# Performance work log

Hardware: AMD Instinct MI355X
Metric: run time of the kernel (lower is better)

Reference implementation:

```python
import jax, jax.numpy as jnp
import numpy as np

A_CONST = 0.1
B_CONST = 0.2
C_CONST = 0.8

INPUT_SIZE = 1024
HIDDEN_SIZE = 2048
BATCH = 32768
SIGMA = 0.02


def acti_func(x, a, b, c):
    # piecewise: a*(1 - x/b) for x<=b ; 0 for b<x<c ; a*(x-c)/(1-c) for x>=c
    low = -a * x / b + a
    high = a * x / (1.0 - c) + a * c / (c - 1.0)
    return jnp.where(x <= b, low, jnp.where(x >= c, high, jnp.zeros_like(x)))


def setup_inputs() -> dict:
    key = jax.random.key(0)
    ks = jax.random.split(key, 4)
    x = jax.random.normal(ks[0], (BATCH, INPUT_SIZE), dtype=jnp.float32)
    W0 = jax.random.normal(ks[1], (INPUT_SIZE, HIDDEN_SIZE), dtype=jnp.float32) * SIGMA
    b0 = jnp.zeros((HIDDEN_SIZE,), dtype=jnp.float32)
    W1 = jax.random.normal(ks[2], (HIDDEN_SIZE, HIDDEN_SIZE), dtype=jnp.float32) * SIGMA
    b1 = jnp.zeros((HIDDEN_SIZE,), dtype=jnp.float32)
    W2 = jax.random.normal(ks[3], (HIDDEN_SIZE, 1), dtype=jnp.float32) * SIGMA
    b2 = jnp.zeros((1,), dtype=jnp.float32)
    return {"x": x, "W0": W0, "b0": b0, "W1": W1, "b1": b1, "W2": W2, "b2": b2}


def reference(x, W0, b0, W1, b1, W2, b2):
    h = jax.nn.elu(x @ W0 + b0)
    h = jax.nn.elu(h @ W1 + b1)
    out = jax.nn.sigmoid(h @ W2 + b2)  # [B, 1]
    alpha = acti_func(out, A_CONST, B_CONST, C_CONST)
    return out, alpha
```

## Files before the change

### kernel.cpp

```cpp
#include <hip/hip_runtime.h>
#include <hip/hip_bf16.h>
#include <stdint.h>

typedef unsigned short u16;
typedef __bf16 bf16x8 __attribute__((ext_vector_type(8)));
typedef float floatx4 __attribute__((ext_vector_type(4)));

__device__ __forceinline__ u16 f2bf(float f) {
  union { float f; unsigned u; } c; c.f = f;
  unsigned r = c.u + 0x7fffu + ((c.u >> 16) & 1u);
  return (u16)(r >> 16);
}

__device__ __forceinline__ void load_lds16(const void* g, void* l) {
  __builtin_amdgcn_global_load_lds(
      (const __attribute__((address_space(1))) void*)g,
      (__attribute__((address_space(3))) void*)l,
      16, 0, 0);
}

__global__ void cast_f32_bf16(const float4* __restrict__ src, ushort4* __restrict__ dst, int n4) {
  int i = blockIdx.x * blockDim.x + threadIdx.x;
  if (i >= n4) return;
  float4 f = src[i];
  ushort4 u;
  u.x = f2bf(f.x); u.y = f2bf(f.y); u.z = f2bf(f.z); u.w = f2bf(f.w);
  dst[i] = u;
}

__global__ void transpose_cast(const float* __restrict__ W, u16* __restrict__ Wt, int R, int C) {
  __shared__ float tile[32][33];
  int bx = blockIdx.x * 32;
  int by = blockIdx.y * 32;
  int tx = threadIdx.x, ty = threadIdx.y;
  #pragma unroll
  for (int i = 0; i < 32; i += 8)
    tile[ty + i][tx] = W[(size_t)(by + ty + i) * C + bx + tx];
  __syncthreads();
  #pragma unroll
  for (int i = 0; i < 32; i += 8)
    Wt[(size_t)(bx + ty + i) * R + by + tx] = f2bf(tile[tx][ty + i]);
}

template<bool FUSE_HEAD>
__global__ __launch_bounds__(256) void gemm_bt_fused(
    const u16* __restrict__ A,
    const u16* __restrict__ Bt,
    const float* __restrict__ bias,
    u16* __restrict__ C,
    const float* __restrict__ W2,
    float* __restrict__ z,
    int M, int N, int K)
{
  __shared__ u16 As[128 * 64];
  __shared__ u16 Bs[128 * 64];

  const int t = threadIdx.x;
  const int w = t >> 6;
  const int l = t & 63;
  const int wm = w >> 1;
  const int wn = w & 1;
  const int lm = l & 15;
  const int q  = l >> 4;

  const int n0 = blockIdx.x * 128;
  const int m0 = blockIdx.y * 128;

  floatx4 acc[4][4];
  #pragma unroll
  for (int i = 0; i < 4; ++i)
    #pragma unroll
    for (int j = 0; j < 4; ++j)
      acc[i][j] = (floatx4){0.f, 0.f, 0.f, 0.f};

  const int rowoff = t >> 3;
  const int lc8 = ((t & 7) ^ (rowoff & 7)) * 8;
  const u16* Ap[4];
  const u16* Bp[4];
  #pragma unroll
  for (int k = 0; k < 4; ++k) {
    Ap[k] = A  + (size_t)(m0 + k * 32 + rowoff) * K + lc8;
    Bp[k] = Bt + (size_t)(n0 + k * 32 + rowoff) * K + lc8;
  }
  const int ldsoff = t * 8;

  const int sw0 = ((0 * 4 + q) ^ (lm & 7)) * 8;
  const int sw1 = ((1 * 4 + q) ^ (lm & 7)) * 8;

  for (int k0 = 0; k0 < K; k0 += 64) {
    __syncthreads();
    #pragma unroll
    for (int k = 0; k < 4; ++k) {
      load_lds16(Ap[k] + k0, &As[k * 2048 + ldsoff]);
      load_lds16(Bp[k] + k0, &Bs[k * 2048 + ldsoff]);
    }
    __syncthreads();

    {
      bf16x8 af[4], bfr[4];
      #pragma unroll
      for (int i = 0; i < 4; ++i)
        af[i] = *(const bf16x8*)(As + (wm * 64 + i * 16 + lm) * 64 + sw0);
      #pragma unroll
      for (int j = 0; j < 4; ++j)
        bfr[j] = *(const bf16x8*)(Bs + (wn * 64 + j * 16 + lm) * 64 + sw0);
      #pragma unroll
      for (int i = 0; i < 4; ++i)
        #pragma unroll
        for (int j = 0; j < 4; ++j)
          acc[i][j] = __builtin_amdgcn_mfma_f32_16x16x32_bf16(af[i], bfr[j], acc[i][j], 0, 0, 0);
    }
    {
      bf16x8 af[4], bfr[4];
      #pragma unroll
      for (int i = 0; i < 4; ++i)
        af[i] = *(const bf16x8*)(As + (wm * 64 + i * 16 + lm) * 64 + sw1);
      #pragma unroll
      for (int j = 0; j < 4; ++j)
        bfr[j] = *(const bf16x8*)(Bs + (wn * 64 + j * 16 + lm) * 64 + sw1);
      #pragma unroll
      for (int i = 0; i < 4; ++i)
        #pragma unroll
        for (int j = 0; j < 4; ++j)
          acc[i][j] = __builtin_amdgcn_mfma_f32_16x16x32_bf16(af[i], bfr[j], acc[i][j], 0, 0, 0);
    }
  }

  float bv[4];
  #pragma unroll
  for (int j = 0; j < 4; ++j) bv[j] = bias[n0 + wn * 64 + j * 16 + lm];

  if (!FUSE_HEAD) {
    #pragma unroll
    for (int i = 0; i < 4; ++i) {
      #pragma unroll
      for (int r = 0; r < 4; ++r) {
        int grow = m0 + wm * 64 + i * 16 + q * 4 + r;
        size_t base = (size_t)grow * N + n0 + wn * 64 + lm;
        #pragma unroll
        for (int j = 0; j < 4; ++j) {
          float v = acc[i][j][r] + bv[j];
          v = v > 0.f ? v : (__expf(v) - 1.f);
          C[base + j * 16] = f2bf(v);
        }
      }
    }
  } else {
    float w2v[4];
    #pragma unroll
    for (int j = 0; j < 4; ++j) w2v[j] = W2[n0 + wn * 64 + j * 16 + lm];
    #pragma unroll
    for (int i = 0; i < 4; ++i) {
      #pragma unroll
      for (int r = 0; r < 4; ++r) {
        float p = 0.f;
        #pragma unroll
        for (int j = 0; j < 4; ++j) {
          float v = acc[i][j][r] + bv[j];
          v = v > 0.f ? v : (__expf(v) - 1.f);
          p += v * w2v[j];
        }
        p += __shfl_xor(p, 1);
        p += __shfl_xor(p, 2);
        p += __shfl_xor(p, 4);
        p += __shfl_xor(p, 8);
        if (lm == 0) atomicAdd(&z[m0 + wm * 64 + i * 16 + q * 4 + r], p);
      }
    }
  }
}

__global__ __launch_bounds__(256) void sigmoid_alpha(
    const float* __restrict__ z, const float* __restrict__ b2,
    float* __restrict__ out, int B)
{
  int i = blockIdx.x * blockDim.x + threadIdx.x;
  if (i >= B) return;
  float o = 1.f / (1.f + expf(-(z[i] + b2[0])));
  float alpha;
  if (o <= 0.2f)      alpha = 0.1f - 0.5f * o;
  else if (o >= 0.8f) alpha = 0.5f * o - 0.4f;
  else                alpha = 0.f;
  out[i] = o;
  out[B + i] = alpha;
}

extern "C" void kernel_launch(void* const* d_in, const int* in_sizes, int n_in,
                              void* d_out, int out_size, void* d_ws, size_t ws_size,
                              hipStream_t stream) {
  const int BATCH = 32768, IN = 1024, HID = 2048;

  const float* x  = (const float*)d_in[0];
  const float* W0 = (const float*)d_in[1];
  const float* b0 = (const float*)d_in[2];
  const float* W1 = (const float*)d_in[3];
  const float* b1 = (const float*)d_in[4];
  const float* W2 = (const float*)d_in[5];
  const float* b2 = (const float*)d_in[6];
  float* out = (float*)d_out;

  char* ws = (char*)d_ws;
  u16* Xb   = (u16*)(ws);
  u16* Wt0  = (u16*)(ws + (size_t)67108864);
  u16* Wt1  = (u16*)(ws + (size_t)71303168);
  u16* h0   = (u16*)(ws + (size_t)79691776);
  float* z  = (float*)(ws + (size_t)213909504);

  {
    int n4 = BATCH * IN / 4;
    cast_f32_bf16<<<n4 / 256, 256, 0, stream>>>((const float4*)x, (ushort4*)Xb, n4);
  }
  transpose_cast<<<dim3(HID / 32, IN / 32), dim3(32, 8), 0, stream>>>(W0, Wt0, IN, HID);
  transpose_cast<<<dim3(HID / 32, HID / 32), dim3(32, 8), 0, stream>>>(W1, Wt1, HID, HID);
  hipMemsetAsync(z, 0, (size_t)BATCH * sizeof(float), stream);
  gemm_bt_fused<false><<<dim3(HID / 128, BATCH / 128), 256, 0, stream>>>(
      Xb, Wt0, b0, h0, nullptr, nullptr, BATCH, HID, IN);
  gemm_bt_fused<true><<<dim3(HID / 128, BATCH / 128), 256, 0, stream>>>(
      h0, Wt1, b1, nullptr, W2, z, BATCH, HID, HID);
  sigmoid_alpha<<<BATCH / 256, 256, 0, stream>>>(z, b2, out, BATCH);
}
```

Measured before the change: 685.5 us.

## Switch GEMM to 32x32x16 MFMA and merge preprocessing into one kernel

The GEMM inner loop now issues 32x32x16 bf16 MFMA instructions on a 2x2 grid of 16-wide accumulators per wave, replacing the 4x4 grid of 16x16x32 ops. This halves the LDS fragment loads per step and uses the larger-tile MFMA shape. The epilogue row mapping and the head reduction change to match the 32x32 output layout. Separately, the input cast, the two weight transpose-casts and the z memset are merged into a single launch to cut launch overhead.

```diff
diff --git a/kernel.cpp b/kernel.cpp
--- a/kernel.cpp
+++ b/kernel.cpp
@@ -4,7 +4,7 @@
 
 typedef unsigned short u16;
 typedef __bf16 bf16x8 __attribute__((ext_vector_type(8)));
-typedef float floatx4 __attribute__((ext_vector_type(4)));
+typedef float floatx16 __attribute__((ext_vector_type(16)));
 
 __device__ __forceinline__ u16 f2bf(float f) {
   union { float f; unsigned u; } c; c.f = f;
@@ -19,27 +19,48 @@
       16, 0, 0);
 }
 
-__global__ void cast_f32_bf16(const float4* __restrict__ src, ushort4* __restrict__ dst, int n4) {
-  int i = blockIdx.x * blockDim.x + threadIdx.x;
-  if (i >= n4) return;
-  float4 f = src[i];
-  ushort4 u;
-  u.x = f2bf(f.x); u.y = f2bf(f.y); u.z = f2bf(f.z); u.w = f2bf(f.w);
-  dst[i] = u;
-}
-
-__global__ void transpose_cast(const float* __restrict__ W, u16* __restrict__ Wt, int R, int C) {
+__global__ __launch_bounds__(256) void preamble(
+    const float* __restrict__ x, const float* __restrict__ W0,
+    const float* __restrict__ W1,
+    u16* __restrict__ Xb, u16* __restrict__ Wt0, u16* __restrict__ Wt1,
+    float* __restrict__ z)
+{
   __shared__ float tile[32][33];
-  int bx = blockIdx.x * 32;
-  int by = blockIdx.y * 32;
-  int tx = threadIdx.x, ty = threadIdx.y;
-  #pragma unroll
-  for (int i = 0; i < 32; i += 8)
-    tile[ty + i][tx] = W[(size_t)(by + ty + i) * C + bx + tx];
-  __syncthreads();
-  #pragma unroll
-  for (int i = 0; i < 32; i += 8)
-    Wt[(size_t)(bx + ty + i) * R + by + tx] = f2bf(tile[tx][ty + i]);
+  const int bid = blockIdx.x;
+  const int t = threadIdx.x;
+
+  if (bid < 32768) {
+    int i = bid * 256 + t;
+    float4 f = ((const float4*)x)[i];
+    ushort4 u;
+    u.x = f2bf(f.x); u.y = f2bf(f.y); u.z = f2bf(f.z); u.w = f2bf(f.w);
+    ((ushort4*)Xb)[i] = u;
+  } else if (bid < 32768 + 2048) {
+    int tb = bid - 32768;
+    int bx = (tb & 63) * 32, by = (tb >> 6) * 32;
+    int tx = t & 31, ty = t >> 5;
+    #pragma unroll
+    for (int i = 0; i < 32; i += 8)
+      tile[ty + i][tx] = W0[(size_t)(by + ty + i) * 2048 + bx + tx];
+    __syncthreads();
+    #pragma unroll
+    for (int i = 0; i < 32; i += 8)
+      Wt0[(size_t)(bx + ty + i) * 1024 + by + tx] = f2bf(tile[tx][ty + i]);
+  } else if (bid < 32768 + 2048 + 4096) {
+    int tb = bid - (32768 + 2048);
+    int bx = (tb & 63) * 32, by = (tb >> 6) * 32;
+    int tx = t & 31, ty = t >> 5;
+    #pragma unroll
+    for (int i = 0; i < 32; i += 8)
+      tile[ty + i][tx] = W1[(size_t)(by + ty + i) * 2048 + bx + tx];
+    __syncthreads();
+    #pragma unroll
+    for (int i = 0; i < 32; i += 8)
+      Wt1[(size_t)(bx + ty + i) * 2048 + by + tx] = f2bf(tile[tx][ty + i]);
+  } else {
+    int tb = bid - (32768 + 2048 + 4096);
+    ((float4*)z)[tb * 256 + t] = (float4){0.f, 0.f, 0.f, 0.f};
+  }
 }
 
 template<bool FUSE_HEAD>
@@ -60,18 +81,18 @@
   const int l = t & 63;
   const int wm = w >> 1;
   const int wn = w & 1;
-  const int lm = l & 15;
-  const int q  = l >> 4;
+  const int lm = l & 31;
+  const int h  = l >> 5;
 
   const int n0 = blockIdx.x * 128;
   const int m0 = blockIdx.y * 128;
 
-  floatx4 acc[4][4];
+  floatx16 acc[2][2];
   #pragma unroll
-  for (int i = 0; i < 4; ++i)
-    #pragma unroll
-    for (int j = 0; j < 4; ++j)
-      acc[i][j] = (floatx4){0.f, 0.f, 0.f, 0.f};
+  for (int i = 0; i < 2; ++i)
+    #pragma unroll
+    for (int j = 0; j < 2; ++j)
+      acc[i][j] = (floatx16)(0.f);
 
   const int rowoff = t >> 3;
   const int lc8 = ((t & 7) ^ (rowoff & 7)) * 8;
@@ -84,8 +105,9 @@
   }
   const int ldsoff = t * 8;
 
-  const int sw0 = ((0 * 4 + q) ^ (lm & 7)) * 8;
-  const int sw1 = ((1 * 4 + q) ^ (lm & 7)) * 8;
+  const int arow0 = (wm * 64 + lm) * 64;
+  const int brow0 = (wn * 64 + lm) * 64;
+  const int swb = (lm & 7);
 
   for (int k0 = 0; k0 < K; k0 += 64) {
     __syncthreads();
@@ -96,66 +118,54 @@
     }
     __syncthreads();
 
-    {
-      bf16x8 af[4], bfr[4];
-      #pragma unroll
-      for (int i = 0; i < 4; ++i)
-        af[i] = *(const bf16x8*)(As + (wm * 64 + i * 16 + lm) * 64 + sw0);
-      #pragma unroll
-      for (int j = 0; j < 4; ++j)
-        bfr[j] = *(const bf16x8*)(Bs + (wn * 64 + j * 16 + lm) * 64 + sw0);
-      #pragma unroll
-      for (int i = 0; i < 4; ++i)
+    #pragma unroll
+    for (int s = 0; s < 4; ++s) {
+      const int sw = ((s * 2 + h) ^ swb) * 8;
+      bf16x8 af[2], bfr[2];
+      #pragma unroll
+      for (int i = 0; i < 2; ++i)
+        af[i] = *(const bf16x8*)(As + arow0 + i * 32 * 64 + sw);
+      #pragma unroll
+      for (int j = 0; j < 2; ++j)
+        bfr[j] = *(const bf16x8*)(Bs + brow0 + j * 32 * 64 + sw);
+      #pragma unroll
+      for (int i = 0; i < 2; ++i)
         #pragma unroll
-        for (int j = 0; j < 4; ++j)
-          acc[i][j] = __builtin_amdgcn_mfma_f32_16x16x32_bf16(af[i], bfr[j], acc[i][j], 0, 0, 0);
-    }
-    {
-      bf16x8 af[4], bfr[4];
-      #pragma unroll
-      for (int i = 0; i < 4; ++i)
-        af[i] = *(const bf16x8*)(As + (wm * 64 + i * 16 + lm) * 64 + sw1);
-      #pragma unroll
-      for (int j = 0; j < 4; ++j)
-        bfr[j] = *(const bf16x8*)(Bs + (wn * 64 + j * 16 + lm) * 64 + sw1);
-      #pragma unroll
-      for (int i = 0; i < 4; ++i)
+        for (int j = 0; j < 2; ++j)
+          acc[i][j] = __builtin_amdgcn_mfma_f32_32x32x16_bf16(af[i], bfr[j], acc[i][j], 0, 0, 0);
+    }
+  }
+
+  float bv[2];
+  #pragma unroll
+  for (int j = 0; j < 2; ++j) bv[j] = bias[n0 + wn * 64 + j * 32 + lm];
+
+  if (!FUSE_HEAD) {
+    #pragma unroll
+    for (int i = 0; i < 2; ++i) {
+      #pragma unroll
+      for (int r = 0; r < 16; ++r) {
+        int row = m0 + wm * 64 + i * 32 + (r & 3) + 8 * (r >> 2) + 4 * h;
+        size_t base = (size_t)row * N + n0 + wn * 64 + lm;
         #pragma unroll
-        for (int j = 0; j < 4; ++j)
-          acc[i][j] = __builtin_amdgcn_mfma_f32_16x16x32_bf16(af[i], bfr[j], acc[i][j], 0, 0, 0);
-    }
-  }
-
-  float bv[4];
-  #pragma unroll
-  for (int j = 0; j < 4; ++j) bv[j] = bias[n0 + wn * 64 + j * 16 + lm];
-
-  if (!FUSE_HEAD) {
-    #pragma unroll
-    for (int i = 0; i < 4; ++i) {
-      #pragma unroll
-      for (int r = 0; r < 4; ++r) {
-        int grow = m0 + wm * 64 + i * 16 + q * 4 + r;
-        size_t base = (size_t)grow * N + n0 + wn * 64 + lm;
-        #pragma unroll
-        for (int j = 0; j < 4; ++j) {
+        for (int j = 0; j < 2; ++j) {
           float v = acc[i][j][r] + bv[j];
           v = v > 0.f ? v : (__expf(v) - 1.f);
-          C[base + j * 16] = f2bf(v);
+          C[base + j * 32] = f2bf(v);
         }
       }
     }
   } else {
-    float w2v[4];
-    #pragma unroll
-    for (int j = 0; j < 4; ++j) w2v[j] = W2[n0 + wn * 64 + j * 16 + lm];
-    #pragma unroll
-    for (int i = 0; i < 4; ++i) {
-      #pragma unroll
-      for (int r = 0; r < 4; ++r) {
+    float w2v[2];
+    #pragma unroll
+    for (int j = 0; j < 2; ++j) w2v[j] = W2[n0 + wn * 64 + j * 32 + lm];
+    #pragma unroll
+    for (int i = 0; i < 2; ++i) {
+      #pragma unroll
+      for (int r = 0; r < 16; ++r) {
         float p = 0.f;
         #pragma unroll
-        for (int j = 0; j < 4; ++j) {
+        for (int j = 0; j < 2; ++j) {
           float v = acc[i][j][r] + bv[j];
           v = v > 0.f ? v : (__expf(v) - 1.f);
           p += v * w2v[j];
@@ -164,7 +174,9 @@
         p += __shfl_xor(p, 2);
         p += __shfl_xor(p, 4);
         p += __shfl_xor(p, 8);
-        if (lm == 0) atomicAdd(&z[m0 + wm * 64 + i * 16 + q * 4 + r], p);
+        p += __shfl_xor(p, 16);
+        if (lm == 0)
+          atomicAdd(&z[m0 + wm * 64 + i * 32 + (r & 3) + 8 * (r >> 2) + 4 * h], p);
       }
     }
   }
@@ -206,13 +218,7 @@
   u16* h0   = (u16*)(ws + (size_t)79691776);
   float* z  = (float*)(ws + (size_t)213909504);
 
-  {
-    int n4 = BATCH * IN / 4;
-    cast_f32_bf16<<<n4 / 256, 256, 0, stream>>>((const float4*)x, (ushort4*)Xb, n4);
-  }
-  transpose_cast<<<dim3(HID / 32, IN / 32), dim3(32, 8), 0, stream>>>(W0, Wt0, IN, HID);
-  transpose_cast<<<dim3(HID / 32, HID / 32), dim3(32, 8), 0, stream>>>(W1, Wt1, HID, HID);
-  hipMemsetAsync(z, 0, (size_t)BATCH * sizeof(float), stream);
+  preamble<<<32768 + 2048 + 4096 + 32, 256, 0, stream>>>(x, W0, W1, Xb, Wt0, Wt1, z);
   gemm_bt_fused<false><<<dim3(HID / 128, BATCH / 128), 256, 0, stream>>>(
       Xb, Wt0, b0, h0, nullptr, nullptr, BATCH, HID, IN);
   gemm_bt_fused<true><<<dim3(HID / 128, BATCH / 128), 256, 0, stream>>>(
```

After: 693.4 us. Within noise of the previous version (+1.2%).
